# Performance work log

Measured on AMD Instinct MI355X. Metric: run time of the kernel, lower is better.

Reference implementation:

```python
import jax, jax.numpy as jnp
import numpy as np

N_SAMPLES, N_HORIZON, N_DOF, N_LINKS = 2048, 128, 7, 9
BASE_MASS, EEF_MASS = 100000.0, 243.66


def _constants():
    mass = jnp.array([105.98, 105.98, 314.98, 279.2, 105.98, 105.98, 243.66], jnp.float32)
    total_mass = jnp.sum(mass) + BASE_MASS + EEF_MASS
    diags = np.array([
        [12.19, 12.19, 3.061],
        [12.19, 12.19, 3.061],
        [15.41, 2094.71, 2103.19],
        [9.522, 1966.28, 1966.28],
        [8.305, 3.061, 8.0386],
        [12.13, 12.13, 3.061],
        [9.336, 44.41, 44.41],
    ], np.float32)
    inertial = jnp.asarray(np.stack([np.diag(d) for d in diags]))  # (7,3,3)
    I0 = jnp.diag(jnp.array([69585.02, 69585.02, 66666.664], jnp.float32))
    # base_com_pose = (tf_link0 @ com_link0_local)[:3,3] * eef_mass/(base+eef)
    base_com = jnp.array([0.0, 0.0, 6.65], jnp.float32) * (243.66 / (100000.0 + 243.66))
    return mass, total_mass, inertial, I0, base_com


def _skew(p):
    # p: (...,3) -> (...,3,3)
    x, y, z = p[..., 0], p[..., 1], p[..., 2]
    o = jnp.zeros_like(x)
    return jnp.stack([
        jnp.stack([o, -z, y], -1),
        jnp.stack([z, o, -x], -1),
        jnp.stack([-y, x, o], -1),
    ], -2)


def _inv3(M):
    # analytic 3x3 inverse (batched)
    a, b, c = M[..., 0, 0], M[..., 0, 1], M[..., 0, 2]
    d, e, f = M[..., 1, 0], M[..., 1, 1], M[..., 1, 2]
    g, h, i = M[..., 2, 0], M[..., 2, 1], M[..., 2, 2]
    A = e * i - f * h
    B = f * g - d * i
    C = d * h - e * g
    det = a * A + b * B + c * C
    inv = jnp.stack([
        jnp.stack([A, c * h - b * i, b * f - c * e], -1),
        jnp.stack([B, a * i - c * g, c * d - a * f], -1),
        jnp.stack([C, b * g - a * h, a * e - b * d], -1),
    ], -2)
    return inv / det[..., None, None]


def setup_inputs() -> dict:
    key = jax.random.key(0)
    k1, k2, k3 = jax.random.split(key, 3)
    com_list = jax.random.normal(k1, (N_SAMPLES, N_HORIZON, 3, N_DOF), jnp.float32)
    link_pose_list = jax.random.normal(k2, (N_SAMPLES, N_HORIZON, 4, 4, N_LINKS), jnp.float32)
    jacobian = jax.random.normal(k3, (N_SAMPLES, N_HORIZON, 6, N_DOF), jnp.float32)
    return {"com_list": com_list, "link_pose_list": link_pose_list, "jacobian": jacobian}


def reference(com_list, link_pose_list, jacobian):
    mass, total_mass, inertial, I0, base_com = _constants()
    tril = jnp.tril(jnp.ones((N_DOF, N_DOF), jnp.float32))
    mass_tril = tril * mass[:, None]  # [i,j] = mass_i if j<=i else 0

    # system COM (mass-weighted manipulator COM over total system mass)
    system_com = jnp.einsum('bhci,i->bhc', com_list, mass) / total_mass  # (b,h,3)
    r_og = system_com - base_com                                          # (b,h,3)
    S_og = _skew(r_og)                                                    # (b,h,3,3)

    Jt = jnp.swapaxes(jacobian[:, :, :3, :], -1, -2)                      # (b,h,j=7,3)
    rp = com_list - link_pose_list[:, :, :3, 3, :N_DOF]                   # (b,h,3,i=7)
    rpt = jnp.swapaxes(rp, -1, -2)                                        # (b,h,i=7,3)

    # cross(J_r[j], r_p[i]) for all (i,j): (b,h,7,7,3)
    cross_all = jnp.cross(Jt[:, :, None, :, :], rpt[:, :, :, None, :])

    # J_tw[c,j] = sum_i mass_tril[i,j] * cross_all[i,j,c]
    J_tw = jnp.einsum('bhijc,ij->bhcj', cross_all, mass_tril)             # (b,h,3,7)

    # (p.p) I - p p^T
    r2 = jnp.sum(r_og * r_og, -1)
    skew_mul = r2[..., None, None] * jnp.eye(3, dtype=r_og.dtype) - r_og[..., :, None] * r_og[..., None, :]
    H_w = jnp.sum(inertial, 0) + jnp.sum(mass) * skew_mul + I0            # (b,h,3,3)

    r_oi = com_list - base_com[:, None]                                   # (b,h,3,7)
    S_oi = _skew(jnp.swapaxes(r_oi, -1, -2))                              # (b,h,7,3,3)

    Hwp1 = jnp.einsum('iad,ij,bhjd->bhaj', inertial, tril, Jt)
    Hwp2 = jnp.einsum('bhiac,bhijc,ij->bhaj', S_oi, cross_all, mass_tril)
    H_theta = Hwp1 + Hwp2 - jnp.einsum('bhij,bhjk->bhik', S_og, J_tw)     # (b,h,3,7)

    H_s = total_mass * jnp.matmul(S_og, S_og) + H_w
    H_s_inv = _inv3(H_s)

    top = -(J_tw / total_mass + jnp.matmul(jnp.matmul(S_og, H_s_inv), H_theta))
    bot = -jnp.matmul(H_s_inv, H_theta)
    return jnp.concatenate([top, bot], axis=-2)                            # (b,h,6,7)
```

## Files before the change

kernel.cpp:

```cpp
#include <hip/hip_runtime.h>

#define TPB 256
#define IPB 256
#define NITEMS (2048*128)

__global__ __launch_bounds__(TPB) void canadarm_kernel(
    const float* __restrict__ com_g,
    const float* __restrict__ pose_g,
    const float* __restrict__ jac_g,
    float* __restrict__ out_g)
{
    __shared__ float lds[IPB*63];
    const int tid = threadIdx.x;
    const size_t item0 = (size_t)blockIdx.x * IPB;

    {
        const float* src = com_g + item0*21;
        #pragma unroll
        for (int k = tid; k < IPB*21; k += TPB) {
            int it = k/21, off = k - it*21;
            lds[it*63 + off] = src[k];
        }
    }
    {
        const float* src = pose_g + item0*144;
        #pragma unroll
        for (int k = tid; k < IPB*21; k += TPB) {
            int it = k/21, idx = k - it*21;
            int r = idx/7, l = idx - r*7;
            lds[it*63 + 21 + idx] = src[it*144 + r*36 + 27 + l];
        }
    }
    {
        const float* src = jac_g + item0*42;
        #pragma unroll
        for (int k = tid; k < IPB*21; k += TPB) {
            int it = k/21, off = k - it*21;
            lds[it*63 + 42 + off] = src[it*42 + off];
        }
    }
    __syncthreads();

    float com[3][7], pp[3][7], J[3][7];
    {
        const float* L = lds + tid*63;
        #pragma unroll
        for (int c = 0; c < 3; ++c)
            #pragma unroll
            for (int i = 0; i < 7; ++i) {
                com[c][i] = L[c*7 + i];
                pp[c][i]  = L[21 + c*7 + i];
                J[c][i]   = L[42 + c*7 + i];
            }
    }
    __syncthreads();

    const float mass[7] = {105.98f,105.98f,314.98f,279.2f,105.98f,105.98f,243.66f};
    const float diag[7][3] = {
        {12.19f,12.19f,3.061f},
        {12.19f,12.19f,3.061f},
        {15.41f,2094.71f,2103.19f},
        {9.522f,1966.28f,1966.28f},
        {8.305f,3.061f,8.0386f},
        {12.13f,12.13f,3.061f},
        {9.336f,44.41f,44.41f}};
    float msum = 0.f;
    #pragma unroll
    for (int i = 0; i < 7; ++i) msum += mass[i];
    const float M_total = msum + 100000.0f + 243.66f;
    const float inv_M   = 1.0f / M_total;
    const float bcz     = 6.65f * (243.66f / (100000.0f + 243.66f));
    float Cd[3];
    #pragma unroll
    for (int a = 0; a < 3; ++a) {
        float s0 = 0.f;
        #pragma unroll
        for (int i = 0; i < 7; ++i) s0 += diag[i][a];
        Cd[a] = s0;
    }
    Cd[0] += 69585.02f; Cd[1] += 69585.02f; Cd[2] += 66666.664f;
    const float Kc = M_total - msum;

    float rg[3];
    #pragma unroll
    for (int c = 0; c < 3; ++c) {
        float s0 = 0.f;
        #pragma unroll
        for (int i = 0; i < 7; ++i) s0 += com[c][i]*mass[i];
        rg[c] = s0 * inv_M;
    }
    rg[2] -= bcz;

    float rp[3][7], roi[3][7];
    #pragma unroll
    for (int i = 0; i < 7; ++i) {
        rp[0][i]  = com[0][i] - pp[0][i];
        rp[1][i]  = com[1][i] - pp[1][i];
        rp[2][i]  = com[2][i] - pp[2][i];
        roi[0][i] = com[0][i];
        roi[1][i] = com[1][i];
        roi[2][i] = com[2][i] - bcz;
    }

    float w0=0.f,w1=0.f,w2=0.f, ssum=0.f;
    float M00=0.f,M01=0.f,M02=0.f,M10=0.f,M11=0.f,M12=0.f,M20=0.f,M21=0.f,M22=0.f;
    float Ds0=0.f, Ds1=0.f, Ds2=0.f;
    float Jtw[3][7], Hth[3][7];
    #pragma unroll
    for (int j = 6; j >= 0; --j) {
        const float mi = mass[j];
        const float ax=rp[0][j],  ay=rp[1][j],  az=rp[2][j];
        const float bx=roi[0][j], by=roi[1][j], bz=roi[2][j];
        w0 += mi*ax; w1 += mi*ay; w2 += mi*az;
        ssum += mi*(ax*bx + ay*by + az*bz);
        M00 += mi*ax*bx; M01 += mi*ax*by; M02 += mi*ax*bz;
        M10 += mi*ay*bx; M11 += mi*ay*by; M12 += mi*ay*bz;
        M20 += mi*az*bx; M21 += mi*az*by; M22 += mi*az*bz;
        Ds0 += diag[j][0]; Ds1 += diag[j][1]; Ds2 += diag[j][2];

        const float jx=J[0][j], jy=J[1][j], jz=J[2][j];
        const float tx = jy*w2 - jz*w1;
        const float ty = jz*w0 - jx*w2;
        const float tz = jx*w1 - jy*w0;
        Jtw[0][j]=tx; Jtw[1][j]=ty; Jtw[2][j]=tz;

        const float h2x = jx*ssum - (M00*jx + M01*jy + M02*jz);
        const float h2y = jy*ssum - (M10*jx + M11*jy + M12*jz);
        const float h2z = jz*ssum - (M20*jx + M21*jy + M22*jz);

        const float cx = rg[1]*tz - rg[2]*ty;
        const float cy = rg[2]*tx - rg[0]*tz;
        const float cz = rg[0]*ty - rg[1]*tx;

        Hth[0][j] = Ds0*jx + h2x - cx;
        Hth[1][j] = Ds1*jy + h2y - cy;
        Hth[2][j] = Ds2*jz + h2z - cz;
    }

    const float r2 = rg[0]*rg[0] + rg[1]*rg[1] + rg[2]*rg[2];
    const float Hs00 = Kc*(rg[0]*rg[0] - r2) + Cd[0];
    const float Hs11 = Kc*(rg[1]*rg[1] - r2) + Cd[1];
    const float Hs22 = Kc*(rg[2]*rg[2] - r2) + Cd[2];
    const float Hs01 = Kc*rg[0]*rg[1];
    const float Hs02 = Kc*rg[0]*rg[2];
    const float Hs12 = Kc*rg[1]*rg[2];
    const float A = Hs11*Hs22 - Hs12*Hs12;
    const float B = Hs12*Hs02 - Hs01*Hs22;
    const float C = Hs01*Hs12 - Hs11*Hs02;
    const float det = Hs00*A + Hs01*B + Hs02*C;
    const float id_ = 1.0f/det;
    const float Hi00 = A*id_, Hi01 = B*id_, Hi02 = C*id_;
    const float Hi11 = (Hs00*Hs22 - Hs02*Hs02)*id_;
    const float Hi12 = (Hs02*Hs01 - Hs00*Hs12)*id_;
    const float Hi22 = (Hs00*Hs11 - Hs01*Hs01)*id_;

    float* O = lds + tid*43;
    #pragma unroll
    for (int j = 0; j < 7; ++j) {
        const float hx=Hth[0][j], hy=Hth[1][j], hz=Hth[2][j];
        const float vx = Hi00*hx + Hi01*hy + Hi02*hz;
        const float vy = Hi01*hx + Hi11*hy + Hi12*hz;
        const float vz = Hi02*hx + Hi12*hy + Hi22*hz;
        const float bx = -vx, by = -vy, bz = -vz;
        O[0*7+j] = -Jtw[0][j]*inv_M + (rg[1]*bz - rg[2]*by);
        O[1*7+j] = -Jtw[1][j]*inv_M + (rg[2]*bx - rg[0]*bz);
        O[2*7+j] = -Jtw[2][j]*inv_M + (rg[0]*by - rg[1]*bx);
        O[3*7+j] = bx;
        O[4*7+j] = by;
        O[5*7+j] = bz;
    }
    __syncthreads();

    {
        float* dst = out_g + item0*42;
        #pragma unroll
        for (int k = tid; k < IPB*42; k += TPB) {
            int it = k/42, off = k - it*42;
            dst[k] = lds[it*43 + off];
        }
    }
}

extern "C" void kernel_launch(void* const* d_in, const int* in_sizes, int n_in,
                              void* d_out, int out_size, void* d_ws, size_t ws_size,
                              hipStream_t stream) {
    const float* com  = (const float*)d_in[0];
    const float* pose = (const float*)d_in[1];
    const float* jac  = (const float*)d_in[2];
    float* out = (float*)d_out;
    dim3 grid(NITEMS/IPB), block(TPB);
    hipLaunchKernelGGL(canadarm_kernel, grid, block, 0, stream, com, pose, jac, out);
}
```

Measured before the change: 270.1 us.

## Use direct global-to-LDS async loads with smaller blocks and float2 stores

Replaces the register-staged global-to-LDS copies with __builtin_amdgcn_global_load_lds, using 16-byte loads for the contiguous com data and 4-byte loads for the strided jacobian and pose slices. Blocks shrink to 64 threads and 64 items, LDS is split into separate per-array regions, and the output is written back as float2 vectors. The aim is to cut VGPR staging and instruction overhead on a bandwidth-bound kernel and to raise occupancy. The LDS addressing of the 16-byte direct loads is intricate, so correctness depends on the per-wave lane layout rules of the builtin.

```diff
diff --git a/kernel.cpp b/kernel.cpp
--- a/kernel.cpp
+++ b/kernel.cpp
@@ -1,8 +1,22 @@
 #include <hip/hip_runtime.h>
 
-#define TPB 256
-#define IPB 256
+#define TPB 64
+#define IPB 64
 #define NITEMS (2048*128)
+
+#define COM0  0
+#define JAC0  (IPB*21)
+#define POSE0 (2*IPB*21)
+#define LDS_FLOATS (3*IPB*21)
+
+__device__ __forceinline__ void gload4(void* lds_dst, const void* gsrc) {
+    __builtin_amdgcn_global_load_lds((const __attribute__((address_space(1))) void*)gsrc,
+                                     (__attribute__((address_space(3))) void*)lds_dst, 4, 0, 0);
+}
+__device__ __forceinline__ void gload16(void* lds_dst, const void* gsrc) {
+    __builtin_amdgcn_global_load_lds((const __attribute__((address_space(1))) void*)gsrc,
+                                     (__attribute__((address_space(3))) void*)lds_dst, 16, 0, 0);
+}
 
 __global__ __launch_bounds__(TPB) void canadarm_kernel(
     const float* __restrict__ com_g,
@@ -10,50 +24,57 @@
     const float* __restrict__ jac_g,
     float* __restrict__ out_g)
 {
-    __shared__ float lds[IPB*63];
+    __shared__ float sh[LDS_FLOATS];
     const int tid = threadIdx.x;
     const size_t item0 = (size_t)blockIdx.x * IPB;
 
     {
         const float* src = com_g + item0*21;
         #pragma unroll
-        for (int k = tid; k < IPB*21; k += TPB) {
-            int it = k/21, off = k - it*21;
-            lds[it*63 + off] = src[k];
+        for (int i = 0; i < 5; ++i) {
+            int s4 = tid + i*64;
+            gload16(&sh[COM0 + (size_t)i*256], src + (size_t)s4*4);
+        }
+        gload4(&sh[COM0 + 1280], src + 1280 + tid);
+    }
+    {
+        const float* src = jac_g + item0*42;
+        #pragma unroll
+        for (int i = 0; i < 21; ++i) {
+            int t  = tid + i*64;
+            int it = t / 21;
+            int off = t - it*21;
+            gload4(&sh[JAC0 + i*64], src + it*42 + off);
         }
     }
     {
         const float* src = pose_g + item0*144;
         #pragma unroll
-        for (int k = tid; k < IPB*21; k += TPB) {
-            int it = k/21, idx = k - it*21;
-            int r = idx/7, l = idx - r*7;
-            lds[it*63 + 21 + idx] = src[it*144 + r*36 + 27 + l];
-        }
-    }
-    {
-        const float* src = jac_g + item0*42;
-        #pragma unroll
-        for (int k = tid; k < IPB*21; k += TPB) {
-            int it = k/21, off = k - it*21;
-            lds[it*63 + 42 + off] = src[it*42 + off];
+        for (int i = 0; i < 21; ++i) {
+            int t   = tid + i*64;
+            int it  = t / 21;
+            int idx = t - it*21;
+            int r   = idx / 7;
+            int l   = idx - r*7;
+            gload4(&sh[POSE0 + i*64], src + it*144 + r*36 + 27 + l);
         }
     }
     __syncthreads();
 
     float com[3][7], pp[3][7], J[3][7];
     {
-        const float* L = lds + tid*63;
+        const float* Lc = sh + COM0  + tid*21;
+        const float* Lj = sh + JAC0  + tid*21;
+        const float* Lp = sh + POSE0 + tid*21;
         #pragma unroll
         for (int c = 0; c < 3; ++c)
             #pragma unroll
             for (int i = 0; i < 7; ++i) {
-                com[c][i] = L[c*7 + i];
-                pp[c][i]  = L[21 + c*7 + i];
-                J[c][i]   = L[42 + c*7 + i];
+                com[c][i] = Lc[c*7 + i];
+                J[c][i]   = Lj[c*7 + i];
+                pp[c][i]  = Lp[c*7 + i];
             }
     }
-    __syncthreads();
 
     const float mass[7] = {105.98f,105.98f,314.98f,279.2f,105.98f,105.98f,243.66f};
     const float diag[7][3] = {
@@ -154,7 +175,9 @@
     const float Hi12 = (Hs02*Hs01 - Hs00*Hs12)*id_;
     const float Hi22 = (Hs00*Hs11 - Hs01*Hs01)*id_;
 
-    float* O = lds + tid*43;
+    __syncthreads();
+
+    float* O = sh + tid*42;
     #pragma unroll
     for (int j = 0; j < 7; ++j) {
         const float hx=Hth[0][j], hy=Hth[1][j], hz=Hth[2][j];
@@ -172,11 +195,12 @@
     __syncthreads();
 
     {
-        float* dst = out_g + item0*42;
-        #pragma unroll
-        for (int k = tid; k < IPB*42; k += TPB) {
-            int it = k/42, off = k - it*42;
-            dst[k] = lds[it*43 + off];
+        const float2* so = (const float2*)sh;
+        float2* dst = (float2*)(out_g + item0*42);
+        #pragma unroll
+        for (int i = 0; i < 21; ++i) {
+            int p = tid + i*64;
+            dst[p] = so[p];
         }
     }
 }
```

Measured after the change: 264.6 us. 1.02x faster.

## Load inputs directly per thread, fuse passes, shrink blocks to one wavefront

Applied to the files above, without the earlier changes.

Drops the cooperative LDS staging of the com, pose and jacobian inputs. Each thread now reads its own item straight from global memory, and the Hth computation is fused into the output loop so the intermediate arrays no longer need to be held. Blocks shrink to 64 threads, and the output is written back through LDS as float2 stores. The cost is uncoalesced strided global reads (stride 21, 144 and 42 floats per lane), which depend on the cache to stay efficient, in exchange for fewer barriers, less LDS and lower register pressure.

```diff
diff --git a/kernel.cpp b/kernel.cpp
--- a/kernel.cpp
+++ b/kernel.cpp
@@ -1,7 +1,6 @@
 #include <hip/hip_runtime.h>
 
-#define TPB 256
-#define IPB 256
+#define TPB 64
 #define NITEMS (2048*128)
 
 __global__ __launch_bounds__(TPB) void canadarm_kernel(
@@ -10,50 +9,18 @@
     const float* __restrict__ jac_g,
     float* __restrict__ out_g)
 {
-    __shared__ float lds[IPB*63];
+    __shared__ float sh[TPB*42];
     const int tid = threadIdx.x;
-    const size_t item0 = (size_t)blockIdx.x * IPB;
+    const size_t item0 = (size_t)blockIdx.x * TPB;
+    const size_t item  = item0 + tid;
 
-    {
-        const float* src = com_g + item0*21;
-        #pragma unroll
-        for (int k = tid; k < IPB*21; k += TPB) {
-            int it = k/21, off = k - it*21;
-            lds[it*63 + off] = src[k];
-        }
-    }
-    {
-        const float* src = pose_g + item0*144;
-        #pragma unroll
-        for (int k = tid; k < IPB*21; k += TPB) {
-            int it = k/21, idx = k - it*21;
-            int r = idx/7, l = idx - r*7;
-            lds[it*63 + 21 + idx] = src[it*144 + r*36 + 27 + l];
-        }
-    }
-    {
-        const float* src = jac_g + item0*42;
-        #pragma unroll
-        for (int k = tid; k < IPB*21; k += TPB) {
-            int it = k/21, off = k - it*21;
-            lds[it*63 + 42 + off] = src[it*42 + off];
-        }
-    }
-    __syncthreads();
+    const float* C  = com_g  + item*21;
+    const float* P  = pose_g + item*144;
+    const float* Jg = jac_g  + item*42;
 
-    float com[3][7], pp[3][7], J[3][7];
-    {
-        const float* L = lds + tid*63;
-        #pragma unroll
-        for (int c = 0; c < 3; ++c)
-            #pragma unroll
-            for (int i = 0; i < 7; ++i) {
-                com[c][i] = L[c*7 + i];
-                pp[c][i]  = L[21 + c*7 + i];
-                J[c][i]   = L[42 + c*7 + i];
-            }
-    }
-    __syncthreads();
+    float com[21];
+    #pragma unroll
+    for (int k = 0; k < 21; ++k) com[k] = C[k];
 
     const float mass[7] = {105.98f,105.98f,314.98f,279.2f,105.98f,105.98f,243.66f};
     const float diag[7][3] = {
@@ -86,56 +53,10 @@
     for (int c = 0; c < 3; ++c) {
         float s0 = 0.f;
         #pragma unroll
-        for (int i = 0; i < 7; ++i) s0 += com[c][i]*mass[i];
+        for (int i = 0; i < 7; ++i) s0 += com[c*7+i]*mass[i];
         rg[c] = s0 * inv_M;
     }
     rg[2] -= bcz;
-
-    float rp[3][7], roi[3][7];
-    #pragma unroll
-    for (int i = 0; i < 7; ++i) {
-        rp[0][i]  = com[0][i] - pp[0][i];
-        rp[1][i]  = com[1][i] - pp[1][i];
-        rp[2][i]  = com[2][i] - pp[2][i];
-        roi[0][i] = com[0][i];
-        roi[1][i] = com[1][i];
-        roi[2][i] = com[2][i] - bcz;
-    }
-
-    float w0=0.f,w1=0.f,w2=0.f, ssum=0.f;
-    float M00=0.f,M01=0.f,M02=0.f,M10=0.f,M11=0.f,M12=0.f,M20=0.f,M21=0.f,M22=0.f;
-    float Ds0=0.f, Ds1=0.f, Ds2=0.f;
-    float Jtw[3][7], Hth[3][7];
-    #pragma unroll
-    for (int j = 6; j >= 0; --j) {
-        const float mi = mass[j];
-        const float ax=rp[0][j],  ay=rp[1][j],  az=rp[2][j];
-        const float bx=roi[0][j], by=roi[1][j], bz=roi[2][j];
-        w0 += mi*ax; w1 += mi*ay; w2 += mi*az;
-        ssum += mi*(ax*bx + ay*by + az*bz);
-        M00 += mi*ax*bx; M01 += mi*ax*by; M02 += mi*ax*bz;
-        M10 += mi*ay*bx; M11 += mi*ay*by; M12 += mi*ay*bz;
-        M20 += mi*az*bx; M21 += mi*az*by; M22 += mi*az*bz;
-        Ds0 += diag[j][0]; Ds1 += diag[j][1]; Ds2 += diag[j][2];
-
-        const float jx=J[0][j], jy=J[1][j], jz=J[2][j];
-        const float tx = jy*w2 - jz*w1;
-        const float ty = jz*w0 - jx*w2;
-        const float tz = jx*w1 - jy*w0;
-        Jtw[0][j]=tx; Jtw[1][j]=ty; Jtw[2][j]=tz;
-
-        const float h2x = jx*ssum - (M00*jx + M01*jy + M02*jz);
-        const float h2y = jy*ssum - (M10*jx + M11*jy + M12*jz);
-        const float h2z = jz*ssum - (M20*jx + M21*jy + M22*jz);
-
-        const float cx = rg[1]*tz - rg[2]*ty;
-        const float cy = rg[2]*tx - rg[0]*tz;
-        const float cz = rg[0]*ty - rg[1]*tx;
-
-        Hth[0][j] = Ds0*jx + h2x - cx;
-        Hth[1][j] = Ds1*jy + h2y - cy;
-        Hth[2][j] = Ds2*jz + h2z - cz;
-    }
 
     const float r2 = rg[0]*rg[0] + rg[1]*rg[1] + rg[2]*rg[2];
     const float Hs00 = Kc*(rg[0]*rg[0] - r2) + Cd[0];
@@ -146,25 +67,66 @@
     const float Hs12 = Kc*rg[1]*rg[2];
     const float A = Hs11*Hs22 - Hs12*Hs12;
     const float B = Hs12*Hs02 - Hs01*Hs22;
-    const float C = Hs01*Hs12 - Hs11*Hs02;
-    const float det = Hs00*A + Hs01*B + Hs02*C;
+    const float Cc = Hs01*Hs12 - Hs11*Hs02;
+    const float det = Hs00*A + Hs01*B + Hs02*Cc;
     const float id_ = 1.0f/det;
-    const float Hi00 = A*id_, Hi01 = B*id_, Hi02 = C*id_;
+    const float Hi00 = A*id_, Hi01 = B*id_, Hi02 = Cc*id_;
     const float Hi11 = (Hs00*Hs22 - Hs02*Hs02)*id_;
     const float Hi12 = (Hs02*Hs01 - Hs00*Hs12)*id_;
     const float Hi22 = (Hs00*Hs11 - Hs01*Hs01)*id_;
 
-    float* O = lds + tid*43;
+    float w0=0.f,w1=0.f,w2=0.f, ssum=0.f;
+    float M00=0.f,M01=0.f,M02=0.f,M10=0.f,M11=0.f,M12=0.f,M20=0.f,M21=0.f,M22=0.f;
+    float Ds0=0.f, Ds1=0.f, Ds2=0.f;
+    float* O = sh + tid*42;
     #pragma unroll
-    for (int j = 0; j < 7; ++j) {
-        const float hx=Hth[0][j], hy=Hth[1][j], hz=Hth[2][j];
+    for (int j = 6; j >= 0; --j) {
+        const float px = P[0*36 + 27 + j];
+        const float py = P[1*36 + 27 + j];
+        const float pz = P[2*36 + 27 + j];
+        const float jx = Jg[0*7 + j];
+        const float jy = Jg[1*7 + j];
+        const float jz = Jg[2*7 + j];
+
+        const float ax = com[0*7+j] - px;
+        const float ay = com[1*7+j] - py;
+        const float az = com[2*7+j] - pz;
+        const float bxr = com[0*7+j];
+        const float byr = com[1*7+j];
+        const float bzr = com[2*7+j] - bcz;
+
+        const float mi = mass[j];
+        w0 += mi*ax; w1 += mi*ay; w2 += mi*az;
+        ssum += mi*(ax*bxr + ay*byr + az*bzr);
+        M00 += mi*ax*bxr; M01 += mi*ax*byr; M02 += mi*ax*bzr;
+        M10 += mi*ay*bxr; M11 += mi*ay*byr; M12 += mi*ay*bzr;
+        M20 += mi*az*bxr; M21 += mi*az*byr; M22 += mi*az*bzr;
+        Ds0 += diag[j][0]; Ds1 += diag[j][1]; Ds2 += diag[j][2];
+
+        const float tx = jy*w2 - jz*w1;
+        const float ty = jz*w0 - jx*w2;
+        const float tz = jx*w1 - jy*w0;
+
+        const float h2x = jx*ssum - (M00*jx + M01*jy + M02*jz);
+        const float h2y = jy*ssum - (M10*jx + M11*jy + M12*jz);
+        const float h2z = jz*ssum - (M20*jx + M21*jy + M22*jz);
+
+        const float cx = rg[1]*tz - rg[2]*ty;
+        const float cy = rg[2]*tx - rg[0]*tz;
+        const float cz = rg[0]*ty - rg[1]*tx;
+
+        const float hx = Ds0*jx + h2x - cx;
+        const float hy = Ds1*jy + h2y - cy;
+        const float hz = Ds2*jz + h2z - cz;
+
         const float vx = Hi00*hx + Hi01*hy + Hi02*hz;
         const float vy = Hi01*hx + Hi11*hy + Hi12*hz;
         const float vz = Hi02*hx + Hi12*hy + Hi22*hz;
         const float bx = -vx, by = -vy, bz = -vz;
-        O[0*7+j] = -Jtw[0][j]*inv_M + (rg[1]*bz - rg[2]*by);
-        O[1*7+j] = -Jtw[1][j]*inv_M + (rg[2]*bx - rg[0]*bz);
-        O[2*7+j] = -Jtw[2][j]*inv_M + (rg[0]*by - rg[1]*bx);
+
+        O[0*7+j] = -tx*inv_M + (rg[1]*bz - rg[2]*by);
+        O[1*7+j] = -ty*inv_M + (rg[2]*bx - rg[0]*bz);
+        O[2*7+j] = -tz*inv_M + (rg[0]*by - rg[1]*bx);
         O[3*7+j] = bx;
         O[4*7+j] = by;
         O[5*7+j] = bz;
@@ -172,11 +134,12 @@
     __syncthreads();
 
     {
-        float* dst = out_g + item0*42;
+        const float2* so = (const float2*)sh;
+        float2* dst = (float2*)(out_g + item0*42);
         #pragma unroll
-        for (int k = tid; k < IPB*42; k += TPB) {
-            int it = k/42, off = k - it*42;
-            dst[k] = lds[it*43 + off];
+        for (int i = 0; i < 21; ++i) {
+            int p = tid + i*64;
+            dst[p] = so[p];
         }
     }
 }
@@ -188,6 +151,6 @@
     const float* pose = (const float*)d_in[1];
     const float* jac  = (const float*)d_in[2];
     float* out = (float*)d_out;
-    dim3 grid(NITEMS/IPB), block(TPB);
+    dim3 grid(NITEMS/TPB), block(TPB);
     hipLaunchKernelGGL(canadarm_kernel, grid, block, 0, stream, com, pose, jac, out);
 }
```

New measurement: 266.7 us. No clear change (-1.2%).
